# Kernel tuning notes

Hardware: AMD Instinct MI355X
Metric: run time of the kernel (lower is better)

Reference implementation:

```python
import jax, jax.numpy as jnp
import numpy as np

ALPHA = 0.3      # robust Welsch scale (hardcoded in calc_chamfer)
EPS = 1e-6       # cosine_similarity eps


def _single_direction(x_points, x_normals, y_points, y_normals):
    """Robust chamfer x->y with K=1 KNN. Returns (mean robust dist, mean normal loss)."""
    # brute-force squared pairwise distances: [B, N, M]
    x2 = jnp.sum(x_points * x_points, axis=-1)            # [B, N]
    y2 = jnp.sum(y_points * y_points, axis=-1)            # [B, M]
    d2 = x2[:, :, None] + y2[:, None, :] - 2.0 * jnp.einsum('bnd,bmd->bnm', x_points, y_points)
    d2 = jnp.maximum(d2, 0.0)
    idx = jnp.argmin(d2, axis=-1)                         # [B, N] nearest neighbor in y
    dists = jnp.take_along_axis(d2, idx[..., None], axis=-1)[..., 0]   # squared dists [B, N]
    # Welsch weight applied to the squared distance (matches torch code), detached
    w = jax.lax.stop_gradient(jnp.exp(-(dists ** 2) / (2.0 * ALPHA * ALPHA)))
    cham_x = jnp.sum(w * dists, axis=1)                   # [B]
    # gather nearest normals and cosine similarity (torch-style per-vector eps clamp)
    yn_near = jnp.take_along_axis(y_normals, idx[..., None], axis=1)   # [B, N, 3]
    xn_norm = jnp.maximum(jnp.linalg.norm(x_normals, axis=-1), EPS)
    yn_norm = jnp.maximum(jnp.linalg.norm(yn_near, axis=-1), EPS)
    cos = jnp.sum(x_normals * yn_near, axis=-1) / (xn_norm * yn_norm)
    cham_norm_x = 1.0 - jnp.abs(cos)                      # abs_cosine=True
    return jnp.mean(cham_x), jnp.mean(cham_norm_x)


def setup_inputs() -> dict:
    key = jax.random.key(0)
    k1, k2, k3, k4 = jax.random.split(key, 4)
    B, N, M = 2, 10000, 10000
    pred_points = jax.random.normal(k1, (B, N, 3), dtype=jnp.float32)
    target_points = jax.random.normal(k2, (B, M, 3), dtype=jnp.float32)
    pn = jax.random.normal(k3, (B, N, 3), dtype=jnp.float32)
    tn = jax.random.normal(k4, (B, M, 3), dtype=jnp.float32)
    pred_normals = pn / jnp.linalg.norm(pn, axis=-1, keepdims=True)
    target_normals = tn / jnp.linalg.norm(tn, axis=-1, keepdims=True)
    return {
        'pred_points': pred_points,
        'pred_normals': pred_normals,
        'target_points': target_points,
        'target_normals': target_normals,
    }


def reference(pred_points, pred_normals, target_points, target_normals):
    # direction 1: target -> pred, direction 2: pred -> target
    d1, n1 = _single_direction(target_points, target_normals, pred_points, pred_normals)
    d2, n2 = _single_direction(pred_points, pred_normals, target_points, target_normals)
    return (d1 + d2, n1 + n2)
```

## Files before the change

### kernel.cpp

```cpp
#include <hip/hip_runtime.h>
#include <math.h>

#define NPTS 10000
#define XPT 4
#define AXCH 10
#define NS 50
#define SLICE 200

__global__ __launch_bounds__(256) void knn_max(
    const float* __restrict__ pred_pts, const float* __restrict__ targ_pts,
    float* __restrict__ wsM)
{
    const int c   = blockIdx.z;
    const int dir = c >> 1, b = c & 1;
    const float* xp = (dir == 0 ? targ_pts : pred_pts) + (size_t)b * NPTS * 3;
    const float* yp = (dir == 0 ? pred_pts : targ_pts) + (size_t)b * NPTS * 3;
    const int s = blockIdx.y;
    const int base = blockIdx.x * (256 * XPT) + threadIdx.x;

    __shared__ float4 sy[SLICE];

    float xx[XPT][3];
#pragma unroll
    for (int k = 0; k < XPT; ++k) {
        const int n = base + k * 256;
        const int nn = (n < NPTS) ? n : (NPTS - 1);
        xx[k][0] = xp[nn * 3 + 0];
        xx[k][1] = xp[nn * 3 + 1];
        xx[k][2] = xp[nn * 3 + 2];
    }
    float best[XPT];
#pragma unroll
    for (int k = 0; k < XPT; ++k) best[k] = -1e30f;

    const int js = s * SLICE;
    for (int j = threadIdx.x; j < SLICE; j += 256) {
        const float a  = yp[(js + j) * 3 + 0];
        const float bb = yp[(js + j) * 3 + 1];
        const float cc = yp[(js + j) * 3 + 2];
        sy[j] = make_float4(a, bb, cc, -0.5f * fmaf(cc, cc, fmaf(bb, bb, a * a)));
    }
    __syncthreads();

#pragma unroll 4
    for (int j = 0; j < SLICE; j += 2) {
        const float4 Y0 = sy[j];
        const float4 Y1 = sy[j + 1];
#pragma unroll
        for (int k = 0; k < XPT; ++k) {
            const float ma = fmaf(xx[k][0], Y0.x,
                             fmaf(xx[k][1], Y0.y,
                             fmaf(xx[k][2], Y0.z, Y0.w)));
            const float mb = fmaf(xx[k][0], Y1.x,
                             fmaf(xx[k][1], Y1.y,
                             fmaf(xx[k][2], Y1.z, Y1.w)));
            best[k] = fmaxf(fmaxf(best[k], ma), mb);
        }
    }

#pragma unroll
    for (int k = 0; k < XPT; ++k) {
        const int n = base + k * 256;
        if (n < NPTS)
            wsM[((size_t)c * NS + s) * NPTS + n] = best[k];
    }
}

__global__ __launch_bounds__(256) void finalize(
    const float* __restrict__ pred_pts, const float* __restrict__ pred_nrm,
    const float* __restrict__ targ_pts, const float* __restrict__ targ_nrm,
    const float* __restrict__ wsM, float2* __restrict__ wsB)
{
    const int c   = blockIdx.y;
    const int dir = c >> 1, b = c & 1;
    const float* xp = (dir == 0 ? targ_pts : pred_pts) + (size_t)b * NPTS * 3;
    const float* xn = (dir == 0 ? targ_nrm : pred_nrm) + (size_t)b * NPTS * 3;
    const float* yp = (dir == 0 ? pred_pts : targ_pts) + (size_t)b * NPTS * 3;
    const float* yn = (dir == 0 ? pred_nrm : targ_nrm) + (size_t)b * NPTS * 3;

    const int lane = threadIdx.x & 7;
    const int n = blockIdx.x * 32 + (threadIdx.x >> 3);

    float t0 = 0.f, t1 = 0.f;
    if (n < NPTS) {
        float bm = -1e30f;
        int   bs = 1 << 30;
        for (int s = lane; s < NS; s += 8) {
            const float m = wsM[((size_t)c * NS + s) * NPTS + n];
            if (m > bm) { bm = m; bs = s; }
        }
#pragma unroll
        for (int w = 1; w < 8; w <<= 1) {
            const float mo = __shfl_xor(bm, w);
            const int   so = __shfl_xor(bs, w);
            if (mo > bm || (mo == bm && so < bs)) { bm = mo; bs = so; }
        }
        const float a  = xp[n * 3 + 0];
        const float bb = xp[n * 3 + 1];
        const float cc = xp[n * 3 + 2];
        const int j0 = bs * SLICE;
        float rb = -1e30f;
        int bidx = 1 << 30;
        for (int j = j0 + lane; j < j0 + SLICE; j += 8) {
            const float ya = yp[j * 3 + 0];
            const float yb = yp[j * 3 + 1];
            const float yc = yp[j * 3 + 2];
            const float hy = -0.5f * fmaf(yc, yc, fmaf(yb, yb, ya * ya));
            const float m  = fmaf(a, ya, fmaf(bb, yb, fmaf(cc, yc, hy)));
            if (m > rb) { rb = m; bidx = j; }
        }
#pragma unroll
        for (int w = 1; w < 8; w <<= 1) {
            const float mo = __shfl_xor(rb, w);
            const int   jo = __shfl_xor(bidx, w);
            if (mo > rb || (mo == rb && jo < bidx)) { rb = mo; bidx = jo; }
        }
        if (lane == 0) {
            const float hx = -0.5f * fmaf(cc, cc, fmaf(bb, bb, a * a));
            float d2 = -2.0f * (rb + hx);
            d2 = fmaxf(d2, 0.0f);
            const float w = __expf(-(d2 * d2) * (1.0f / 0.18f));
            t0 = w * d2;
            const float nx0 = xn[n * 3 + 0], nx1 = xn[n * 3 + 1], nx2 = xn[n * 3 + 2];
            const float ny0 = yn[(size_t)bidx * 3 + 0];
            const float ny1 = yn[(size_t)bidx * 3 + 1];
            const float ny2 = yn[(size_t)bidx * 3 + 2];
            const float nnx = fmaxf(sqrtf(nx0 * nx0 + nx1 * nx1 + nx2 * nx2), 1e-6f);
            const float nny = fmaxf(sqrtf(ny0 * ny0 + ny1 * ny1 + ny2 * ny2), 1e-6f);
            const float cosv = (nx0 * ny0 + nx1 * ny1 + nx2 * ny2) / (nnx * nny);
            t1 = 1.0f - fabsf(cosv);
        }
    }

    __shared__ float r0[256], r1[256];
    r0[threadIdx.x] = t0;
    r1[threadIdx.x] = t1;
    __syncthreads();
    for (int st = 128; st > 0; st >>= 1) {
        if (threadIdx.x < st) {
            r0[threadIdx.x] += r0[threadIdx.x + st];
            r1[threadIdx.x] += r1[threadIdx.x + st];
        }
        __syncthreads();
    }
    if (threadIdx.x == 0)
        wsB[blockIdx.y * gridDim.x + blockIdx.x] = make_float2(r0[0], r1[0]);
}

__global__ __launch_bounds__(256) void reduce_final(
    const float2* __restrict__ wsB, int nblocks, float* __restrict__ out)
{
    __shared__ float r0[256], r1[256];
    const int t = threadIdx.x;
    float s0 = 0.f, s1 = 0.f;
    for (int i = t; i < nblocks; i += 256) {
        const float2 v = wsB[i];
        s0 += v.x;
        s1 += v.y;
    }
    r0[t] = s0; r1[t] = s1;
    __syncthreads();
    for (int st = 128; st > 0; st >>= 1) {
        if (t < st) { r0[t] += r0[t + st]; r1[t] += r1[t + st]; }
        __syncthreads();
    }
    if (t == 0) {
        out[0] = 0.5f * r0[0];
        out[1] = r1[0] * (1.0f / 20000.0f);
    }
}

extern "C" void kernel_launch(void* const* d_in, const int* in_sizes, int n_in,
                              void* d_out, int out_size, void* d_ws, size_t ws_size,
                              hipStream_t stream)
{
    const float* pred_pts = (const float*)d_in[0];
    const float* pred_nrm = (const float*)d_in[1];
    const float* targ_pts = (const float*)d_in[2];
    const float* targ_nrm = (const float*)d_in[3];
    float* out = (float*)d_out;

    const int BXCH = (NPTS + 31) / 32;

    float* wsM = (float*)d_ws;
    float2* wsB = (float2*)((char*)d_ws + (size_t)4 * NS * NPTS * sizeof(float));

    dim3 gA(AXCH, NS, 4);
    knn_max<<<gA, 256, 0, stream>>>(pred_pts, targ_pts, wsM);

    dim3 gB(BXCH, 4);
    finalize<<<gB, 256, 0, stream>>>(pred_pts, pred_nrm, targ_pts, targ_nrm,
                                     wsM, wsB);

    reduce_final<<<1, 256, 0, stream>>>(wsB, BXCH * 4, out);
}
```

Before: 49.48 us.

## Use fewer, larger candidate slices with tiled LDS staging and wider finalize groups

Cuts the number of target slices from 50 to 10, each 1000 points wide. Each knn_max block now loops over two 500-point LDS tiles, so the per-slice partial-max workspace shrinks fivefold and the first kernel launches fewer blocks. The finalize kernel switches to 16 lanes per query point, so each lane reads one slice max directly, then rescans a 1000-point winning slice instead of 200 points. The trade-off is fewer blocks in the first kernel, which lowers parallelism, and a longer exact rescan per query in finalize.

```diff
diff --git a/kernel.cpp b/kernel.cpp
--- a/kernel.cpp
+++ b/kernel.cpp
@@ -4,8 +4,9 @@
 #define NPTS 10000
 #define XPT 4
 #define AXCH 10
-#define NS 50
-#define SLICE 200
+#define NS 10
+#define SLICE 1000
+#define TILE 500
 
 __global__ __launch_bounds__(256) void knn_max(
     const float* __restrict__ pred_pts, const float* __restrict__ targ_pts,
@@ -18,7 +19,7 @@
     const int s = blockIdx.y;
     const int base = blockIdx.x * (256 * XPT) + threadIdx.x;
 
-    __shared__ float4 sy[SLICE];
+    __shared__ float4 sy[TILE];
 
     float xx[XPT][3];
 #pragma unroll
@@ -33,28 +34,31 @@
 #pragma unroll
     for (int k = 0; k < XPT; ++k) best[k] = -1e30f;
 
-    const int js = s * SLICE;
-    for (int j = threadIdx.x; j < SLICE; j += 256) {
-        const float a  = yp[(js + j) * 3 + 0];
-        const float bb = yp[(js + j) * 3 + 1];
-        const float cc = yp[(js + j) * 3 + 2];
-        sy[j] = make_float4(a, bb, cc, -0.5f * fmaf(cc, cc, fmaf(bb, bb, a * a)));
-    }
-    __syncthreads();
-
+    const int jstart = s * SLICE, jend = jstart + SLICE;
+    for (int t0 = jstart; t0 < jend; t0 += TILE) {
+        __syncthreads();
+        for (int j = threadIdx.x; j < TILE; j += 256) {
+            const float a  = yp[(t0 + j) * 3 + 0];
+            const float bb = yp[(t0 + j) * 3 + 1];
+            const float cc = yp[(t0 + j) * 3 + 2];
+            sy[j] = make_float4(a, bb, cc,
+                                -0.5f * fmaf(cc, cc, fmaf(bb, bb, a * a)));
+        }
+        __syncthreads();
 #pragma unroll 4
-    for (int j = 0; j < SLICE; j += 2) {
-        const float4 Y0 = sy[j];
-        const float4 Y1 = sy[j + 1];
-#pragma unroll
-        for (int k = 0; k < XPT; ++k) {
-            const float ma = fmaf(xx[k][0], Y0.x,
-                             fmaf(xx[k][1], Y0.y,
-                             fmaf(xx[k][2], Y0.z, Y0.w)));
-            const float mb = fmaf(xx[k][0], Y1.x,
-                             fmaf(xx[k][1], Y1.y,
-                             fmaf(xx[k][2], Y1.z, Y1.w)));
-            best[k] = fmaxf(fmaxf(best[k], ma), mb);
+        for (int j = 0; j < TILE; j += 2) {
+            const float4 Y0 = sy[j];
+            const float4 Y1 = sy[j + 1];
+#pragma unroll
+            for (int k = 0; k < XPT; ++k) {
+                const float ma = fmaf(xx[k][0], Y0.x,
+                                 fmaf(xx[k][1], Y0.y,
+                                 fmaf(xx[k][2], Y0.z, Y0.w)));
+                const float mb = fmaf(xx[k][0], Y1.x,
+                                 fmaf(xx[k][1], Y1.y,
+                                 fmaf(xx[k][2], Y1.z, Y1.w)));
+                best[k] = fmaxf(fmaxf(best[k], ma), mb);
+            }
         }
     }
 
@@ -78,21 +82,21 @@
     const float* yp = (dir == 0 ? pred_pts : targ_pts) + (size_t)b * NPTS * 3;
     const float* yn = (dir == 0 ? pred_nrm : targ_nrm) + (size_t)b * NPTS * 3;
 
-    const int lane = threadIdx.x & 7;
-    const int n = blockIdx.x * 32 + (threadIdx.x >> 3);
+    const int lane = threadIdx.x & 15;
+    const int n = blockIdx.x * 16 + (threadIdx.x >> 4);
 
     float t0 = 0.f, t1 = 0.f;
     if (n < NPTS) {
         float bm = -1e30f;
         int   bs = 1 << 30;
-        for (int s = lane; s < NS; s += 8) {
-            const float m = wsM[((size_t)c * NS + s) * NPTS + n];
-            if (m > bm) { bm = m; bs = s; }
-        }
-#pragma unroll
-        for (int w = 1; w < 8; w <<= 1) {
-            const float mo = __shfl_xor(bm, w);
-            const int   so = __shfl_xor(bs, w);
+        if (lane < NS) {
+            bm = wsM[((size_t)c * NS + lane) * NPTS + n];
+            bs = lane;
+        }
+#pragma unroll
+        for (int w = 1; w < 16; w <<= 1) {
+            const float mo = __shfl_xor(bm, w, 16);
+            const int   so = __shfl_xor(bs, w, 16);
             if (mo > bm || (mo == bm && so < bs)) { bm = mo; bs = so; }
         }
         const float a  = xp[n * 3 + 0];
@@ -101,7 +105,7 @@
         const int j0 = bs * SLICE;
         float rb = -1e30f;
         int bidx = 1 << 30;
-        for (int j = j0 + lane; j < j0 + SLICE; j += 8) {
+        for (int j = j0 + lane; j < j0 + SLICE; j += 16) {
             const float ya = yp[j * 3 + 0];
             const float yb = yp[j * 3 + 1];
             const float yc = yp[j * 3 + 2];
@@ -110,9 +114,9 @@
             if (m > rb) { rb = m; bidx = j; }
         }
 #pragma unroll
-        for (int w = 1; w < 8; w <<= 1) {
-            const float mo = __shfl_xor(rb, w);
-            const int   jo = __shfl_xor(bidx, w);
+        for (int w = 1; w < 16; w <<= 1) {
+            const float mo = __shfl_xor(rb, w, 16);
+            const int   jo = __shfl_xor(bidx, w, 16);
             if (mo > rb || (mo == rb && jo < bidx)) { rb = mo; bidx = jo; }
         }
         if (lane == 0) {
@@ -180,7 +184,7 @@
     const float* targ_nrm = (const float*)d_in[3];
     float* out = (float*)d_out;
 
-    const int BXCH = (NPTS + 31) / 32;
+    const int BXCH = (NPTS + 15) / 16;
 
     float* wsM = (float*)d_ws;
     float2* wsB = (float2*)((char*)d_ws + (size_t)4 * NS * NPTS * sizeof(float));
```

Measured after the change: 80.99 us. +63.7%, slower.
